# Kernel tuning notes

Hardware: AMD Instinct MI355X
Metric: run time of the kernel (lower is better)

## Reference

```python
import jax, jax.numpy as jnp
import numpy as np

N = 8192; S = 32; EMB = 256; NH = 8; HD = EMB // NH; NT = 4; K = 2; L = 2; E = 131072
IN_DIMS = [128, 64, 32, 16]; COUNTS = [4096, 2048, 1024, 1024]
BETA = 1.0; TEMPER = 1.0; SLOPE = 0.2; LN_EPS = 1e-5


def setup_inputs() -> dict:
    key = jax.random.key(0)
    ks = iter(jax.random.split(key, 64))
    def nrm(shape, scale=1.0):
        return jax.random.normal(next(ks), shape, jnp.float32) * scale
    inp = {}
    for i, (d, c) in enumerate(zip(IN_DIMS, COUNTS)):
        inp[f"feat{i}"] = nrm((c, d))
        inp[f"Wfc{i}"] = nrm((d, EMB), d ** -0.5)
        inp[f"bfc{i}"] = nrm((EMB,), 0.01)
    inp["type_emb"] = nrm((NT, NT))
    inp["Wgcn"] = nrm((K, EMB, EMB), EMB ** -0.5)
    inp["bgcn"] = nrm((K, EMB), 0.01)
    inp["Wre"] = nrm((K, NT, NT), NT ** -0.5)
    inp["bre"] = nrm((K, NT), 0.01)
    inp["wtre"] = jnp.ones((K, NT), jnp.float32)
    inp["Wl"] = nrm((L, EMB, EMB), EMB ** -0.5)
    inp["Wr"] = nrm((L, EMB, EMB), EMB ** -0.5)
    inp["al"] = nrm((L, HD), HD ** -0.5)
    inp["ar"] = nrm((L, HD), HD ** -0.5)
    inp["Wrs"] = nrm((L, NT, NT * NH), NT ** -0.5)
    inp["Wrt"] = nrm((L, NT, NT * NH), NT ** -0.5)
    inp["Wfin"] = nrm((L, EMB, EMB), EMB ** -0.5)
    inp["ln_g"] = jnp.ones((L, EMB), jnp.float32)
    inp["ln_b"] = jnp.zeros((L, EMB), jnp.float32)
    inp["src"] = jax.random.randint(next(ks), (E,), 0, N)
    inp["dst"] = jax.random.randint(next(ks), (E,), 0, N)
    inp["node_type"] = jnp.concatenate([jnp.full((c,), t, jnp.int32) for t, c in enumerate(COUNTS)])
    inp["seqs"] = jax.random.randint(next(ks), (N, S), 0, N)
    return inp


def _l2n(x):
    return x / jnp.maximum(jnp.linalg.norm(x, axis=1, keepdims=True), 1e-12)


def _ln(x, g, b):
    m = x.mean(-1, keepdims=True)
    v = ((x - m) ** 2).mean(-1, keepdims=True)
    return (x - m) * jax.lax.rsqrt(v + LN_EPS) * g + b


def _agt(h, rh, Wl_, Wr_, al_, ar_, Wrs_, Wrt_, Wfin_, g_, b_):
    B, Sq, _ = h.shape
    fl = (h @ Wl_).reshape(B, Sq, NH, HD).transpose(0, 2, 1, 3)  # [B,NH,S,HD]
    fr = (h @ Wr_).reshape(B, Sq, NH, HD).transpose(0, 2, 1, 3)
    sl = jnp.einsum('bhsd,d->bhs', jax.nn.leaky_relu(fl, SLOPE), al_)
    sr = jnp.einsum('bhsd,d->bhs', jax.nn.leaky_relu(fr, SLOPE), ar_)
    score = sl[:, :, :, None] + sr[:, :, None, :]  # [B,NH,S,S]
    rk = (rh @ Wrs_).reshape(B, Sq, NH, NT).transpose(0, 2, 1, 3)  # [B,NH,S,NT]
    rq = (rh @ Wrt_).reshape(B, Sq, NH, NT).transpose(0, 2, 1, 3)
    score = score + BETA * jnp.einsum('bhir,bhjr->bhij', rk, rq)
    attn = jax.nn.softmax(score / TEMPER, axis=-1)
    ctx = jnp.einsum('bhij,bhjd->bhid', attn, fr)
    h_sa = ctx.transpose(0, 2, 1, 3).reshape(B, Sq, EMB)
    return _ln(h + h_sa @ Wfin_, g_, b_)


def reference(feat0, feat1, feat2, feat3, Wfc0, bfc0, Wfc1, bfc1, Wfc2, bfc2, Wfc3, bfc3,
              type_emb, Wgcn, bgcn, Wre, bre, wtre, Wl, Wr, al, ar, Wrs, Wrt, Wfin, ln_g, ln_b,
              src, dst, node_type, seqs):
    feats = [feat0, feat1, feat2, feat3]
    Wfcs = [Wfc0, Wfc1, Wfc2, Wfc3]
    bfcs = [bfc0, bfc1, bfc2, bfc3]
    gh = jnp.concatenate([f @ W + b for f, W, b in zip(feats, Wfcs, bfcs)], axis=0)  # [N,EMB]
    Nn = gh.shape[0]
    loop = jnp.arange(Nn, dtype=src.dtype)  # self-loops (graph.add_self_loop)
    src_f = jnp.concatenate([src, loop]); dst_f = jnp.concatenate([dst, loop])
    ones = jnp.ones(src_f.shape[0], jnp.float32)
    outdeg = jnp.clip(jax.ops.segment_sum(ones, src_f, num_segments=Nn), 1.0)
    indeg = jnp.clip(jax.ops.segment_sum(ones, dst_f, num_segments=Nn), 1.0)
    n_out = outdeg ** -0.5; n_in = indeg ** -0.5
    ret = [_l2n(gh)]
    R = type_emb[node_type]  # [N,NT]
    for k in range(K):
        # GraphConv, norm='both', relu
        x = (gh * n_out[:, None]) @ Wgcn[k]
        gh = jax.nn.relu(jax.ops.segment_sum(x[src_f], dst_f, num_segments=Nn) * n_in[:, None] + bgcn[k])
        # REConv: left norm, weight, per-node type scale, scatter-sum, right norm, bias, relu
        r = ((R * n_out[:, None]) @ Wre[k]) * wtre[k][node_type][:, None]
        R = jax.nn.relu(jax.ops.segment_sum(r[src_f], dst_f, num_segments=Nn) * n_in[:, None] + bre[k])
    h = gh[seqs]   # [N,S,EMB]
    rh = R[seqs]   # [N,S,NT]
    for l in range(L):
        h = _agt(h, rh, Wl[l], Wr[l], al[l], ar[l], Wrs[l], Wrt[l], Wfin[l], ln_g[l], ln_b[l])
        ret.append(_l2n(h[:, 0, :]))
    return jnp.concatenate(ret, axis=1)  # [N, EMB*(1+L)]
```

## Files before the change

### kernel.cpp

```cpp
#include <hip/hip_runtime.h>
#include <hip/hip_bf16.h>
#include <cstdint>
#include <cstddef>

typedef unsigned short ushortT;
typedef unsigned int uintT;

using bf16x8 = __attribute__((ext_vector_type(8))) short;
using f32x4  = __attribute__((ext_vector_type(4))) float;

static constexpr int NN  = 8192;
static constexpr int EE  = 131072;
static constexpr float SLOPE  = 0.2f;
static constexpr float LN_EPS = 1e-5f;

#define DEVI __device__ __forceinline__

DEVI float red32(float v) {
  #pragma unroll
  for (int m = 16; m >= 1; m >>= 1) v += __shfl_xor(v, m, 64);
  return v;
}
DEVI float red64(float v) {
  #pragma unroll
  for (int m = 32; m >= 1; m >>= 1) v += __shfl_xor(v, m, 64);
  return v;
}
DEVI float max32(float v) {
  #pragma unroll
  for (int m = 16; m >= 1; m >>= 1) v = fmaxf(v, __shfl_xor(v, m, 64));
  return v;
}
DEVI float blo(uintT u) { union { uintT i; float f; } c; c.i = u << 16; return c.f; }
DEVI float bhi(uintT u) { union { uintT i; float f; } c; c.i = u & 0xffff0000u; return c.f; }
DEVI float b2f(ushortT u) { union { uintT i; float f; } c; c.i = ((uintT)u) << 16; return c.f; }
DEVI ushortT f2bu(float f) {
  __hip_bfloat16 h = __float2bfloat16(f);
  return *reinterpret_cast<ushortT*>(&h);
}
DEVI void storeC(float* p, float v) { *p = v; }
DEVI void storeC(ushortT* p, float v) { *p = f2bu(v); }

__global__ __launch_bounds__(256) void fc_kernel(
    const float* __restrict__ f0, const float* __restrict__ f1,
    const float* __restrict__ f2, const float* __restrict__ f3,
    const float* __restrict__ w0, const float* __restrict__ w1,
    const float* __restrict__ w2, const float* __restrict__ w3,
    const float* __restrict__ b0, const float* __restrict__ b1,
    const float* __restrict__ b2, const float* __restrict__ b3,
    float* __restrict__ gh, float* __restrict__ out)
{
  const int nb = blockIdx.x * 32;
  const int t  = threadIdx.x;
  int base, D;
  const float *F, *W, *Bv;
  if (nb < 4096)      { base = 0;    D = 128; F = f0; W = w0; Bv = b0; }
  else if (nb < 6144) { base = 4096; D = 64;  F = f1; W = w1; Bv = b1; }
  else if (nb < 7168) { base = 6144; D = 32;  F = f2; W = w2; Bv = b2; }
  else                { base = 7168; D = 16;  F = f3; W = w3; Bv = b3; }

  __shared__ float Fs[32 * 128];
  __shared__ float red[32][4];
  __shared__ float nrm[32];

  const int total = 32 * D;
  for (int i = t; i < total; i += 256) Fs[i] = F[(size_t)(nb - base) * D + i];
  __syncthreads();

  float acc[32];
  #pragma unroll
  for (int r = 0; r < 32; ++r) acc[r] = Bv[t];
  for (int d = 0; d < D; ++d) {
    float w = W[(size_t)d * 256 + t];
    #pragma unroll
    for (int r = 0; r < 32; ++r) acc[r] = fmaf(Fs[r * D + d], w, acc[r]);
  }

  const int lane = t & 63, wid = t >> 6;
  #pragma unroll
  for (int r = 0; r < 32; ++r) {
    float v = acc[r] * acc[r];
    for (int o = 32; o > 0; o >>= 1) v += __shfl_down(v, o, 64);
    if (lane == 0) red[r][wid] = v;
  }
  __syncthreads();
  if (t < 32) {
    float s = red[t][0] + red[t][1] + red[t][2] + red[t][3];
    nrm[t] = 1.0f / fmaxf(sqrtf(s), 1e-12f);
  }
  __syncthreads();
  #pragma unroll
  for (int r = 0; r < 32; ++r) {
    gh[(size_t)(nb + r) * 256 + t]  = acc[r];
    out[(size_t)(nb + r) * 768 + t] = acc[r] * nrm[r];
  }
}

__global__ __launch_bounds__(256) void zero_counts(int* outc, int* inc) {
  int g = blockIdx.x * 256 + threadIdx.x;
  if (g < NN) outc[g] = 0; else inc[g - NN] = 0;
}
__global__ __launch_bounds__(256) void count_deg(const int* __restrict__ src,
                                                 const int* __restrict__ dst,
                                                 int* outc, int* inc) {
  int g = blockIdx.x * 256 + threadIdx.x;
  atomicAdd(&outc[src[g]], 1);
  atomicAdd(&inc[dst[g]], 1);
}
__global__ __launch_bounds__(256) void norm_kernel(const int* __restrict__ outc,
                                                   const int* __restrict__ inc,
                                                   float* n_out, float* n_in) {
  int g = blockIdx.x * 256 + threadIdx.x;
  n_out[g] = rsqrtf((float)outc[g] + 1.0f);
  n_in[g]  = rsqrtf((float)inc[g] + 1.0f);
}
__global__ __launch_bounds__(1024) void scan_kernel(const int* __restrict__ inc,
                                                    int* __restrict__ offs) {
  __shared__ int sums[1024];
  const int t = threadIdx.x;
  int x[8];
  const int base = t * 8;
  int s = 0;
  #pragma unroll
  for (int i = 0; i < 8; ++i) { int v = inc[base + i] + 1; x[i] = s; s += v; }
  sums[t] = s;
  __syncthreads();
  for (int off = 1; off < 1024; off <<= 1) {
    int a = (t >= off) ? sums[t - off] : 0;
    __syncthreads();
    sums[t] += a;
    __syncthreads();
  }
  const int pre = (t > 0) ? sums[t - 1] : 0;
  #pragma unroll
  for (int i = 0; i < 8; ++i) offs[base + i] = pre + x[i];
  if (t == 1023) offs[NN] = sums[1023];
}
__global__ __launch_bounds__(256) void copy_cur(const int* __restrict__ offs, int* cur) {
  int g = blockIdx.x * 256 + threadIdx.x;
  cur[g] = offs[g];
}
__global__ __launch_bounds__(256) void fill_csr(const int* __restrict__ src,
                                                const int* __restrict__ dst,
                                                int* cur, int* __restrict__ csr) {
  int g = blockIdx.x * 256 + threadIdx.x;
  int s, d;
  if (g < EE) { s = src[g]; d = dst[g]; }
  else        { s = g - EE; d = g - EE; }
  int pos = atomicAdd(&cur[d], 1);
  csr[pos] = s;
}
__global__ __launch_bounds__(256) void init_R(const float* __restrict__ type_emb,
                                              const int* __restrict__ nt,
                                              float* __restrict__ R) {
  int g = blockIdx.x * 256 + threadIdx.x;
  int n = g >> 2, c = g & 3;
  R[g] = type_emb[nt[n] * 4 + c];
}

template<bool ROWSCALE, bool STORE, bool RED, typename CT>
__global__ __launch_bounds__(256) void mfma_gemm_kernel(
    const float* __restrict__ A, const float* __restrict__ W,
    const float* __restrict__ rowscale,
    CT* __restrict__ C, const float* __restrict__ avec,
    float* __restrict__ SSo)
{
  const int m0 = blockIdx.x * 64;
  const int n0 = blockIdx.y * 64;
  const int t = threadIdx.x;
  const int w = t >> 6, l = t & 63;
  const int wr = w >> 1, wc = w & 1;
  const int l15 = l & 15, l16 = l >> 4;

  __shared__ alignas(16) ushortT As[64][72];
  __shared__ alignas(16) ushortT Bs[64][72];

  f32x4 acc[2][2];
  #pragma unroll
  for (int mh = 0; mh < 2; ++mh)
    #pragma unroll
    for (int nh = 0; nh < 2; ++nh)
      #pragma unroll
      for (int r = 0; r < 4; ++r) acc[mh][nh][r] = 0.f;

  for (int k0 = 0; k0 < 256; k0 += 64) {
    #pragma unroll
    for (int rep = 0; rep < 16; ++rep) {
      int flat = rep * 256 + t;
      int r = flat >> 6, k = flat & 63;
      float v = A[(size_t)(m0 + r) * 256 + k0 + k];
      if constexpr (ROWSCALE) v *= rowscale[m0 + r];
      As[r][k] = f2bu(v);
    }
    #pragma unroll
    for (int rep = 0; rep < 16; ++rep) {
      int flat = rep * 256 + t;
      int k = flat >> 6, n = flat & 63;
      Bs[n][k] = f2bu(W[(size_t)(k0 + k) * 256 + n0 + n]);
    }
    __syncthreads();
    #pragma unroll
    for (int ks = 0; ks < 2; ++ks) {
      const int kb = ks * 32 + l16 * 8;
      bf16x8 afr[2], bfr[2];
      #pragma unroll
      for (int mh = 0; mh < 2; ++mh)
        afr[mh] = *reinterpret_cast<const bf16x8*>(&As[wr * 32 + mh * 16 + l15][kb]);
      #pragma unroll
      for (int nh = 0; nh < 2; ++nh)
        bfr[nh] = *reinterpret_cast<const bf16x8*>(&Bs[wc * 32 + nh * 16 + l15][kb]);
      #pragma unroll
      for (int mh = 0; mh < 2; ++mh)
        #pragma unroll
        for (int nh = 0; nh < 2; ++nh)
          acc[mh][nh] = __builtin_amdgcn_mfma_f32_16x16x32_bf16(
              afr[mh], bfr[nh], acc[mh][nh], 0, 0, 0);
    }
    __syncthreads();
  }
  if constexpr (STORE) {
    #pragma unroll
    for (int mh = 0; mh < 2; ++mh)
      #pragma unroll
      for (int nh = 0; nh < 2; ++nh)
        #pragma unroll
        for (int r = 0; r < 4; ++r) {
          const int row = m0 + wr * 32 + mh * 16 + l16 * 4 + r;
          const int col = n0 + wc * 32 + nh * 16 + l15;
          storeC(&C[(size_t)row * 256 + col], acc[mh][nh][r]);
        }
  }
  if constexpr (RED) {
    const float av0 = avec[l15], av1 = avec[16 + l15];
    #pragma unroll
    for (int mh = 0; mh < 2; ++mh)
      #pragma unroll
      for (int r = 0; r < 4; ++r) {
        float s = 0.f;
        {
          float x = acc[mh][0][r];
          s = fmaf(x > 0.f ? x : SLOPE * x, av0, s);
          x = acc[mh][1][r];
          s = fmaf(x > 0.f ? x : SLOPE * x, av1, s);
        }
        #pragma unroll
        for (int m = 8; m >= 1; m >>= 1) s += __shfl_xor(s, m, 64);
        if (l15 == 0) {
          const int row = m0 + wr * 32 + mh * 16 + l16 * 4 + r;
          SSo[(size_t)row * 8 + blockIdx.y * 2 + wc] = s;
        }
      }
  }
}

__global__ __launch_bounds__(256) void agg2_kernel(
    const int* __restrict__ offs, const int* __restrict__ csr,
    const ushortT* __restrict__ X, const float* __restrict__ n_in,
    const float* __restrict__ bias, float* __restrict__ ghn,
    ushortT* __restrict__ ghb)
{
  const int n  = blockIdx.x * 2 + (threadIdx.x >> 7);
  const int tc = threadIdx.x & 127;
  const uintT* X2 = reinterpret_cast<const uintT*>(X);
  const int s0 = offs[n], s1 = offs[n + 1];
  float a0 = 0.f, a1 = 0.f;
  for (int i = s0; i < s1; ++i) {
    const uintT u = X2[(size_t)csr[i] * 128 + tc];
    a0 += blo(u);
    a1 += bhi(u);
  }
  const float ni = n_in[n];
  const float g0 = fmaxf(fmaf(a0, ni, bias[2 * tc]), 0.f);
  const float g1 = fmaxf(fmaf(a1, ni, bias[2 * tc + 1]), 0.f);
  float2 g2; g2.x = g0; g2.y = g1;
  reinterpret_cast<float2*>(ghn)[(size_t)n * 128 + tc] = g2;
  if (ghb)
    reinterpret_cast<uintT*>(ghb)[(size_t)n * 128 + tc] =
        (uintT)f2bu(g0) | ((uintT)f2bu(g1) << 16);
}

__global__ __launch_bounds__(256) void re_proj(
    const float* __restrict__ R, const float* __restrict__ n_out,
    const float* __restrict__ Wre, const float* __restrict__ wtre,
    const int* __restrict__ nt, float* __restrict__ rtmp)
{
  int g = blockIdx.x * 256 + threadIdx.x;
  int n = g >> 2, j = g & 3;
  float s = 0.f;
  #pragma unroll
  for (int c = 0; c < 4; ++c) s += R[n * 4 + c] * Wre[c * 4 + j];
  rtmp[g] = s * n_out[n] * wtre[nt[n]];
}
__global__ __launch_bounds__(256) void re_agg(
    const int* __restrict__ offs, const int* __restrict__ csr,
    const float* __restrict__ rtmp, const float* __restrict__ n_in,
    const float* __restrict__ bre, float* __restrict__ Rn)
{
  int g = blockIdx.x * 256 + threadIdx.x;
  int n = g >> 2, j = g & 3;
  float a = 0.f;
  for (int i = offs[n]; i < offs[n + 1]; ++i) a += rtmp[csr[i] * 4 + j];
  Rn[g] = fmaxf(fmaf(a, n_in[n], bre[j]), 0.f);
}
__global__ __launch_bounds__(256) void rkq_kernel(
    const float* __restrict__ R, const float* __restrict__ Wrs,
    const float* __restrict__ Wrt, float* __restrict__ RKQ)
{
  int g = blockIdx.x * 256 + threadIdx.x;
  int n = g >> 7, c = g & 127;
  int which = c >> 5, cc = c & 31;
  const float* Wp = (which == 0) ? Wrs : (which == 1) ? Wrt
                   : (which == 2) ? (Wrs + 128) : (Wrt + 128);
  float s = 0.f;
  #pragma unroll
  for (int r = 0; r < 4; ++r) s += R[n * 4 + r] * Wp[r * 32 + cc];
  RKQ[g] = s;
}

__global__ __launch_bounds__(256) void vec4_kernel(
    const float* __restrict__ ln_g, const float* __restrict__ ln_b,
    const float* __restrict__ Wr2, float* __restrict__ vecs)
{
  const int which = blockIdx.x, t = threadIdx.x;
  const float* s = (which & 1) ? ln_b : ln_g;
  float a = 0.f;
  for (int k = 0; k < 256; ++k) a = fmaf(s[k], Wr2[(size_t)k * 256 + t], a);
  vecs[which * 256 + t] = a;
}
__global__ __launch_bounds__(256) void wg2i_kernel(
    const float* __restrict__ ln_g, const float* __restrict__ Wr2,
    ushortT* __restrict__ Wg2i)
{
  const int gid = blockIdx.x * 256 + threadIdx.x;
  const int ks  = gid >> 10;
  const int cgl = (gid >> 6) & 15;
  const int l   = gid & 63;
  const int col = cgl * 16 + (l & 15);
  const int kb  = ks * 32 + (l >> 4) * 8;
  ushortT v[8];
  #pragma unroll
  for (int e = 0; e < 8; ++e)
    v[e] = f2bu(ln_g[kb + e] * Wr2[(size_t)(kb + e) * 256 + col]);
  *reinterpret_cast<bf16x8*>(&Wg2i[(size_t)gid * 8]) =
      *reinterpret_cast<const bf16x8*>(v);
}
__global__ __launch_bounds__(256) void wl2b_kernel(
    const float* __restrict__ Wl2, ushortT* __restrict__ Wl2b)
{
  int g = blockIdx.x * 256 + threadIdx.x;
  Wl2b[g] = f2bu(Wl2[g]);
}

__global__ __launch_bounds__(256) void mega7_kernel(
    const int* __restrict__ seqs,
    const ushortT* __restrict__ ghb,
    const ushortT* __restrict__ GW,
    const float* __restrict__ SLg, const float* __restrict__ SRg,
    const float* __restrict__ RKQ,
    const float* __restrict__ vecs,
    const ushortT* __restrict__ Wg2i,
    const ushortT* __restrict__ Wl2b,
    const float* __restrict__ al2, const float* __restrict__ ar2,
    const float* __restrict__ ln_g, const float* __restrict__ ln_b,
    float* __restrict__ h1r0buf, float* __restrict__ ctx2buf,
    float* __restrict__ out)
{
  __shared__ int idx[32];
  __shared__ alignas(16) ushortT bufA[10240];
  __shared__ alignas(16) ushortT bufB[10240];
  __shared__ float SRs[8][32];
  __shared__ float RQs[32][36];
  __shared__ float rk2s[32];
  __shared__ float part[32][4], partq[32][4];
  __shared__ float mu_s[32], rs_s[32];
  __shared__ float SR2s[8][32];
  __shared__ float sl2s[8];
  __shared__ float scp[8][32];
  __shared__ float h1r0s[256];
  __shared__ float wred4[4];
  __shared__ float nrm1s;

  const int b = blockIdx.x, t = threadIdx.x;
  const int h8 = t >> 5, lo = t & 31;
  const int w = t >> 6, l = t & 63;
  const int l15 = l & 15, l16 = l >> 4;

  if (t < 32) idx[t] = seqs[b * 32 + t];
  __syncthreads();

  const float sli = SLg[(size_t)idx[lo] * 8 + h8];
  const float rk0 = RKQ[(size_t)idx[lo] * 128 + h8 * 4 + 0];
  const float rk1 = RKQ[(size_t)idx[lo] * 128 + h8 * 4 + 1];
  const float rk2_ = RKQ[(size_t)idx[lo] * 128 + h8 * 4 + 2];
  const float rk3 = RKQ[(size_t)idx[lo] * 128 + h8 * 4 + 3];

  {
    const uintT* GWu = reinterpret_cast<const uintT*>(GW);
    #pragma unroll
    for (int rep = 0; rep < 16; ++rep) {
      int flat = rep * 256 + t;
      int j = flat >> 7, cp = flat & 127;
      const uintT u = GWu[(size_t)idx[j] * 128 + cp];
      const int rA = 2 * cp;
      const int k = (rA >> 3) & 3;
      const int off = (((j >> 3) ^ k) << 3) + (j & 7);
      bufA[rA * 40 + off]       = (ushortT)(u & 0xffffu);
      bufA[(rA + 1) * 40 + off] = (ushortT)(u >> 16);
    }
  }
  SRs[h8][lo] = SRg[(size_t)idx[lo] * 8 + h8];
  #pragma unroll
  for (int rep = 0; rep < 4; ++rep) {
    int flat = rep * 256 + t, s3 = flat >> 5, c3 = flat & 31;
    RQs[s3][c3] = RKQ[(size_t)idx[s3] * 128 + 32 + c3];
  }
  if (t < 32) rk2s[t] = RKQ[(size_t)idx[0] * 128 + 64 + t];
  __syncthreads();

  {
    float p1[32];
    float m = -1e30f;
    #pragma unroll
    for (int j = 0; j < 32; ++j) {
      float sc = sli + SRs[h8][j]
               + rk0 * RQs[j][h8 * 4 + 0] + rk1 * RQs[j][h8 * 4 + 1]
               + rk2_ * RQs[j][h8 * 4 + 2] + rk3 * RQs[j][h8 * 4 + 3];
      p1[j] = sc; m = fmaxf(m, sc);
    }
    float sum = 0.f;
    #pragma unroll
    for (int j = 0; j < 32; ++j) { p1[j] = __expf(p1[j] - m); sum += p1[j]; }
    const float inv = 1.f / sum;
    const int row = t;
    const int k = (row >> 3) & 3;
    uintT* pw = reinterpret_cast<uintT*>(bufB) + row * 20;
    #pragma unroll
    for (int o = 0; o < 4; ++o) {
      uint4 v;
      v.x = (uintT)f2bu(p1[8 * o + 0] * inv) | ((uintT)f2bu(p1[8 * o + 1] * inv) << 16);
      v.y = (uintT)f2bu(p1[8 * o + 2] * inv) | ((uintT)f2bu(p1[8 * o + 3] * inv) << 16);
      v.z = (uintT)f2bu(p1[8 * o + 4] * inv) | ((uintT)f2bu(p1[8 * o + 5] * inv) << 16);
      v.w = (uintT)f2bu(p1[8 * o + 6] * inv) | ((uintT)f2bu(p1[8 * o + 7] * inv) << 16);
      *reinterpret_cast<uint4*>(pw + ((o ^ k) << 2)) = v;
    }
  }
  __syncthreads();

  int irow[2][4];
  #pragma unroll
  for (int mh = 0; mh < 2; ++mh)
    #pragma unroll
    for (int r = 0; r < 4; ++r)
      irow[mh][r] = idx[mh * 16 + l16 * 4 + r];

  bf16x8 af[2][2];
  #pragma unroll
  for (int hh = 0; hh < 2; ++hh) {
    const int h = 2 * w + hh;
    #pragma unroll
    for (int mh = 0; mh < 2; ++mh) {
      const int row = h * 32 + mh * 16 + l15;
      const int k = (row >> 3) & 3;
      af[hh][mh] = *reinterpret_cast<const bf16x8*>(&bufB[row * 40 + ((l16 ^ k) << 3)]);
    }
  }

  f32x4 acc[2][2][2];
  #pragma unroll
  for (int hh = 0; hh < 2; ++hh) {
    const int h = 2 * w + hh;
    bf16x8 bf[2];
    #pragma unroll
    for (int nh = 0; nh < 2; ++nh) {
      const int row = h * 32 + nh * 16 + l15;
      const int k = (row >> 3) & 3;
      bf[nh] = *reinterpret_cast<const bf16x8*>(&bufA[row * 40 + ((l16 ^ k) << 3)]);
    }
    #pragma unroll
    for (int mh = 0; mh < 2; ++mh)
      #pragma unroll
      for (int nh = 0; nh < 2; ++nh) {
        f32x4 z = {0.f, 0.f, 0.f, 0.f};
        acc[hh][mh][nh] = __builtin_amdgcn_mfma_f32_16x16x32_bf16(af[hh][mh], bf[nh], z, 0, 0, 0);
      }
  }
  {
    float sum_[2][4], sq_[2][4];
    #pragma unroll
    for (int mh = 0; mh < 2; ++mh)
      #pragma unroll
      for (int r = 0; r < 4; ++r) { sum_[mh][r] = 0.f; sq_[mh][r] = 0.f; }
    #pragma unroll
    for (int hh = 0; hh < 2; ++hh)
      #pragma unroll
      for (int mh = 0; mh < 2; ++mh)
        #pragma unroll
        for (int nh = 0; nh < 2; ++nh) {
          const int col = (2 * w + hh) * 32 + nh * 16 + l15;
          #pragma unroll
          for (int r = 0; r < 4; ++r) {
            float v = acc[hh][mh][nh][r] + b2f(ghb[(size_t)irow[mh][r] * 256 + col]);
            acc[hh][mh][nh][r] = v;
            sum_[mh][r] += v;
            sq_[mh][r] = fmaf(v, v, sq_[mh][r]);
          }
        }
    #pragma unroll
    for (int mh = 0; mh < 2; ++mh)
      #pragma unroll
      for (int r = 0; r < 4; ++r) {
        float s = sum_[mh][r], q = sq_[mh][r];
        #pragma unroll
        for (int m = 8; m >= 1; m >>= 1) {
          s += __shfl_xor(s, m, 64);
          q += __shfl_xor(q, m, 64);
        }
        if (l15 == 0) {
          part[mh * 16 + l16 * 4 + r][w]  = s;
          partq[mh * 16 + l16 * 4 + r][w] = q;
        }
      }
    if (l16 == 0) {
      #pragma unroll
      for (int hh = 0; hh < 2; ++hh)
        #pragma unroll
        for (int nh = 0; nh < 2; ++nh)
          h1r0s[(2 * w + hh) * 32 + nh * 16 + l15] = acc[hh][0][nh][0];
    }
  }
  __syncthreads();

  if (t < 32) {
    float sm = part[t][0] + part[t][1] + part[t][2] + part[t][3];
    float sq = partq[t][0] + partq[t][1] + partq[t][2] + partq[t][3];
    const float m = sm * (1.f / 256.f);
    const float v = fmaxf(sq * (1.f / 256.f) - m * m, 0.f);
    mu_s[t] = m;
    rs_s[t] = rsqrtf(v + LN_EPS);
  }
  __syncthreads();

  #pragma unroll
  for (int hh = 0; hh < 2; ++hh)
    #pragma unroll
    for (int mh = 0; mh < 2; ++mh)
      #pragma unroll
      for (int nh = 0; nh < 2; ++nh) {
        const int col = (2 * w + hh) * 32 + nh * 16 + l15;
        #pragma unroll
        for (int r = 0; r < 4; ++r) {
          const int row = mh * 16 + l16 * 4 + r;
          bufB[row * 264 + col] = f2bu(acc[hh][mh][nh][r]);
        }
      }
  #pragma unroll
  for (int rep = 0; rep < 4; ++rep) {
    int flat = rep * 256 + t, s3 = flat >> 5, c3 = flat & 31;
    RQs[s3][c3] = RKQ[(size_t)idx[s3] * 128 + 96 + c3];
  }
  {
    const float mu0 = mu_s[0], rs0 = rs_s[0];
    float hv = fmaf((h1r0s[t] - mu0) * rs0, ln_g[t], ln_b[t]);
    h1r0buf[(size_t)b * 256 + t] = hv;
    float sq = red64(hv * hv);
    h1r0s[t] = hv;
    if ((t & 63) == 0) wred4[t >> 6] = sq;
  }
  __syncthreads();

  if (t == 0) nrm1s = 1.f / fmaxf(sqrtf(wred4[0] + wred4[1] + wred4[2] + wred4[3]), 1e-12f);

  {
    f32x4 acc2[2][4];
    #pragma unroll
    for (int mh = 0; mh < 2; ++mh)
      #pragma unroll
      for (int cg = 0; cg < 4; ++cg)
        #pragma unroll
        for (int r = 0; r < 4; ++r) acc2[mh][cg][r] = 0.f;
    #pragma unroll
    for (int ks = 0; ks < 8; ++ks) {
      const int ko = ks * 32 + l16 * 8;
      bf16x8 a2[2];
      #pragma unroll
      for (int mh = 0; mh < 2; ++mh)
        a2[mh] = *reinterpret_cast<const bf16x8*>(&bufB[(mh * 16 + l15) * 264 + ko]);
      #pragma unroll
      for (int cg = 0; cg < 4; ++cg) {
        const bf16x8 b2 = *reinterpret_cast<const bf16x8*>(
            &Wg2i[((size_t)(ks * 16 + (w * 4 + cg)) * 64 + l) * 8]);
        #pragma unroll
        for (int mh = 0; mh < 2; ++mh)
          acc2[mh][cg] = __builtin_amdgcn_mfma_f32_16x16x32_bf16(a2[mh], b2, acc2[mh][cg], 0, 0, 0);
      }
    }
    float rsv[2][4], rmv[2][4];
    #pragma unroll
    for (int mh = 0; mh < 2; ++mh)
      #pragma unroll
      for (int r = 0; r < 4; ++r) {
        const int row = mh * 16 + l16 * 4 + r;
        rsv[mh][r] = rs_s[row];
        rmv[mh][r] = rsv[mh][r] * mu_s[row];
      }
    float sacc[2][2][4];
    #pragma unroll
    for (int hh = 0; hh < 2; ++hh)
      #pragma unroll
      for (int mh = 0; mh < 2; ++mh)
        #pragma unroll
        for (int r = 0; r < 4; ++r) sacc[hh][mh][r] = 0.f;
    float ar2v[2] = { ar2[l15], ar2[16 + l15] };
    #pragma unroll
    for (int cg = 0; cg < 4; ++cg) {
      const int col = w * 64 + cg * 16 + l15;
      const float v1c = vecs[col], v2c = vecs[256 + col];
      const int hh = cg >> 1;
      #pragma unroll
      for (int mh = 0; mh < 2; ++mh)
        #pragma unroll
        for (int r = 0; r < 4; ++r) {
          const int row = mh * 16 + l16 * 4 + r;
          float fa = fmaf(rsv[mh][r], acc2[mh][cg][r], fmaf(-rmv[mh][r], v1c, v2c));
          bufA[row * 268 + col] = f2bu(fa);
          float lr = fa > 0.f ? fa : SLOPE * fa;
          sacc[hh][mh][r] = fmaf(lr, ar2v[cg & 1], sacc[hh][mh][r]);
        }
    }
    #pragma unroll
    for (int hh = 0; hh < 2; ++hh)
      #pragma unroll
      for (int mh = 0; mh < 2; ++mh)
        #pragma unroll
        for (int r = 0; r < 4; ++r) {
          float s = sacc[hh][mh][r];
          #pragma unroll
          for (int m = 8; m >= 1; m >>= 1) s += __shfl_xor(s, m, 64);
          if (l15 == 0) SR2s[2 * w + hh][mh * 16 + l16 * 4 + r] = s;
        }
  }
  {
    float fl = 0.f;
    #pragma unroll 8
    for (int k = 0; k < 256; ++k)
      fl = fmaf(h1r0s[k], b2f(Wl2b[(size_t)k * 256 + t]), fl);
    float lr = (fl > 0.f ? fl : SLOPE * fl) * al2[lo];
    lr = red32(lr);
    if (lo == 0) sl2s[h8] = lr;
  }
  __syncthreads();

  {
    float s2 = sl2s[h8] + SR2s[h8][lo]
             + rk2s[h8 * 4 + 0] * RQs[lo][h8 * 4 + 0]
             + rk2s[h8 * 4 + 1] * RQs[lo][h8 * 4 + 1]
             + rk2s[h8 * 4 + 2] * RQs[lo][h8 * 4 + 2]
             + rk2s[h8 * 4 + 3] * RQs[lo][h8 * 4 + 3];
    const float m2 = max32(s2);
    const float e = __expf(s2 - m2);
    const float su = red32(e);
    scp[h8][lo] = e / su;
  }
  __syncthreads();

  {
    float a = 0.f;
    #pragma unroll
    for (int j = 0; j < 32; ++j) a = fmaf(scp[h8][j], b2f(bufA[j * 268 + t]), a);
    ctx2buf[(size_t)b * 256 + t] = a;
  }
  out[(size_t)b * 768 + 256 + t] = h1r0s[t] * nrm1s;
}

__global__ __launch_bounds__(256) void ln_l2n_kernel(
    const float* __restrict__ Y, const float* __restrict__ res,
    const float* __restrict__ lng, const float* __restrict__ lnb,
    float* __restrict__ out)
{
  const int row = blockIdx.x, t = threadIdx.x;
  __shared__ float s4[4], q4[4];
  const float y = Y[(size_t)row * 256 + t] + res[(size_t)row * 256 + t];
  float s = red64(y);
  float q = red64(y * y);
  if ((t & 63) == 0) { s4[t >> 6] = s; q4[t >> 6] = q; }
  __syncthreads();
  const float mu = (s4[0] + s4[1] + s4[2] + s4[3]) * (1.f / 256.f);
  const float var = fmaxf((q4[0] + q4[1] + q4[2] + q4[3]) * (1.f / 256.f) - mu * mu, 0.f);
  const float rstd = rsqrtf(var + LN_EPS);
  const float yn = fmaf((y - mu) * rstd, lng[t], lnb[t]);
  float nq = red64(yn * yn);
  __syncthreads();
  if ((t & 63) == 0) s4[t >> 6] = nq;
  __syncthreads();
  const float nrm = 1.f / fmaxf(sqrtf(s4[0] + s4[1] + s4[2] + s4[3]), 1e-12f);
  out[(size_t)row * 768 + 512 + t] = yn * nrm;
}

extern "C" void kernel_launch(void* const* d_in, const int* in_sizes, int n_in,
                              void* d_out, int out_size, void* d_ws, size_t ws_size,
                              hipStream_t stream)
{
  (void)in_sizes; (void)n_in; (void)out_size; (void)ws_size;

  const float* feat[4]; const float* wfc[4]; const float* bfc[4];
  for (int i = 0; i < 4; ++i) {
    feat[i] = (const float*)d_in[i * 3 + 0];
    wfc[i]  = (const float*)d_in[i * 3 + 1];
    bfc[i]  = (const float*)d_in[i * 3 + 2];
  }
  const float* type_emb = (const float*)d_in[12];
  const float* Wgcn = (const float*)d_in[13];
  const float* bgcn = (const float*)d_in[14];
  const float* Wre  = (const float*)d_in[15];
  const float* bre  = (const float*)d_in[16];
  const float* wtre = (const float*)d_in[17];
  const float* Wl   = (const float*)d_in[18];
  const float* Wr   = (const float*)d_in[19];
  const float* al   = (const float*)d_in[20];
  const float* ar   = (const float*)d_in[21];
  const float* Wrs  = (const float*)d_in[22];
  const float* Wrt  = (const float*)d_in[23];
  const float* Wfin = (const float*)d_in[24];
  const float* ln_g = (const float*)d_in[25];
  const float* ln_b = (const float*)d_in[26];
  const int* src       = (const int*)d_in[27];
  const int* dst       = (const int*)d_in[28];
  const int* node_type = (const int*)d_in[29];
  const int* seqs      = (const int*)d_in[30];
  float* out = (float*)d_out;

  char* p = (char*)d_ws;
  auto take = [&](size_t n) { char* q = p; p += (n + 255) & ~(size_t)255; return q; };
  float* gh    = (float*)take((size_t)NN * 256 * 4);
  float* Xf    = (float*)take((size_t)NN * 256 * 4);
  float* GR1   = (float*)take((size_t)NN * 256 * 4);
  float* RKQ   = (float*)take((size_t)NN * 128 * 4);
  float* SLg   = (float*)take((size_t)NN * 8 * 4);
  float* SRg   = (float*)take((size_t)NN * 8 * 4);
  float* n_out = (float*)take((size_t)NN * 4);
  float* n_in_ = (float*)take((size_t)NN * 4);
  int*   outc  = (int*)take((size_t)NN * 4);
  int*   inc   = (int*)take((size_t)NN * 4);
  int*   offs  = (int*)take((size_t)(NN + 1) * 4);
  int*   cur   = (int*)take((size_t)NN * 4);
  int*   csr   = (int*)take((size_t)(EE + NN) * 4);
  float* R     = (float*)take((size_t)NN * 4 * 4);
  float* rtmp  = (float*)take((size_t)NN * 4 * 4);
  ushortT* GW   = (ushortT*)take((size_t)NN * 256 * 2);
  ushortT* ghb  = (ushortT*)take((size_t)NN * 256 * 2);
  ushortT* Xb   = (ushortT*)take((size_t)NN * 256 * 2);
  ushortT* Wg2i = (ushortT*)take((size_t)131072 * 2);
  ushortT* Wl2b = (ushortT*)take((size_t)65536 * 2);
  float* vecs  = (float*)take((size_t)2 * 256 * 4);
  float* ctx2buf = Xf;
  float* h1r0buf = GR1;
  float* Yb      = gh;

  const float* Wr2 = Wr + 65536;
  const float* Wl2 = Wl + 65536;

  fc_kernel<<<256, 256, 0, stream>>>(feat[0], feat[1], feat[2], feat[3],
                                     wfc[0], wfc[1], wfc[2], wfc[3],
                                     bfc[0], bfc[1], bfc[2], bfc[3], gh, out);
  zero_counts<<<64, 256, 0, stream>>>(outc, inc);
  count_deg<<<512, 256, 0, stream>>>(src, dst, outc, inc);
  norm_kernel<<<32, 256, 0, stream>>>(outc, inc, n_out, n_in_);
  scan_kernel<<<1, 1024, 0, stream>>>(inc, offs);
  copy_cur<<<32, 256, 0, stream>>>(offs, cur);
  fill_csr<<<544, 256, 0, stream>>>(src, dst, cur, csr);
  init_R<<<128, 256, 0, stream>>>(type_emb, node_type, R);

  vec4_kernel<<<2, 256, 0, stream>>>(ln_g, ln_b, Wr2, vecs);
  wg2i_kernel<<<64, 256, 0, stream>>>(ln_g, Wr2, Wg2i);
  wl2b_kernel<<<256, 256, 0, stream>>>(Wl2, Wl2b);

  for (int k = 0; k < 2; ++k) {
    mfma_gemm_kernel<true, true, false, ushortT>
        <<<dim3(128, 4), 256, 0, stream>>>(gh, Wgcn + (size_t)k * 65536,
                                           n_out, Xb, nullptr, nullptr);
    agg2_kernel<<<NN / 2, 256, 0, stream>>>(offs, csr, Xb, n_in_,
                                            bgcn + k * 256, gh,
                                            k == 1 ? ghb : nullptr);
    re_proj<<<128, 256, 0, stream>>>(R, n_out, Wre + k * 16, wtre + k * 4, node_type, rtmp);
    re_agg<<<128, 256, 0, stream>>>(offs, csr, rtmp, n_in_, bre + k * 4, R);
  }

  rkq_kernel<<<4096, 256, 0, stream>>>(R, Wrs, Wrt, RKQ);
  mfma_gemm_kernel<false, false, true, float>
      <<<dim3(128, 4), 256, 0, stream>>>(gh, Wl, nullptr, (float*)nullptr, al, SLg);
  mfma_gemm_kernel<false, true, true, float>
      <<<dim3(128, 4), 256, 0, stream>>>(gh, Wr, nullptr, GR1, ar, SRg);
  mfma_gemm_kernel<false, true, false, ushortT>
      <<<dim3(128, 4), 256, 0, stream>>>(GR1, Wfin, nullptr, GW, nullptr, nullptr);

  mega7_kernel<<<NN, 256, 0, stream>>>(seqs, ghb, GW, SLg, SRg, RKQ, vecs,
                                       Wg2i, Wl2b,
                                       al + 32, ar + 32, ln_g, ln_b,
                                       h1r0buf, ctx2buf, out);

  mfma_gemm_kernel<false, true, false, float>
      <<<dim3(128, 4), 256, 0, stream>>>(ctx2buf, Wfin + 65536, nullptr,
                                         Yb, nullptr, nullptr);
  ln_l2n_kernel<<<NN, 256, 0, stream>>>(Yb, h1r0buf, ln_g + 256, ln_b + 256, out);
}
```

Before: 572.7 us.

## Fuse final Wfin GEMM and LayerNorm into mega kernel; merge Wl/Wr GEMMs and small setup kernels

The final layer's Wfin projection, residual add, LayerNorm and L2 normalisation move into the per-sequence mega kernel. Each block does a 256x256 matrix-vector product in FP32 FMAs against bf16 weights, which removes the separate MFMA GEMM, the LN kernel and their intermediate buffers. The Wl and Wr projections become one MFMA kernel that shares the A tile, and norm and copy_cur are folded into the scan kernel. The cost is that every mega-kernel block now streams the whole 128KB Wfin2 matrix through a scalar matvec. This is likely served from L2, but it adds serial compute to each block.

```diff
diff --git a/kernel.cpp b/kernel.cpp
--- a/kernel.cpp
+++ b/kernel.cpp
@@ -107,15 +107,11 @@
   atomicAdd(&outc[src[g]], 1);
   atomicAdd(&inc[dst[g]], 1);
 }
-__global__ __launch_bounds__(256) void norm_kernel(const int* __restrict__ outc,
-                                                   const int* __restrict__ inc,
-                                                   float* n_out, float* n_in) {
-  int g = blockIdx.x * 256 + threadIdx.x;
-  n_out[g] = rsqrtf((float)outc[g] + 1.0f);
-  n_in[g]  = rsqrtf((float)inc[g] + 1.0f);
-}
-__global__ __launch_bounds__(1024) void scan_kernel(const int* __restrict__ inc,
-                                                    int* __restrict__ offs) {
+__global__ __launch_bounds__(1024) void scan_kernel(
+    const int* __restrict__ inc, const int* __restrict__ outc,
+    int* __restrict__ offs, int* __restrict__ cur,
+    float* __restrict__ n_out, float* __restrict__ n_in)
+{
   __shared__ int sums[1024];
   const int t = threadIdx.x;
   int x[8];
@@ -133,12 +129,14 @@
   }
   const int pre = (t > 0) ? sums[t - 1] : 0;
   #pragma unroll
-  for (int i = 0; i < 8; ++i) offs[base + i] = pre + x[i];
+  for (int i = 0; i < 8; ++i) {
+    const int o = pre + x[i];
+    offs[base + i] = o;
+    cur[base + i]  = o;
+    n_in[base + i]  = rsqrtf((float)inc[base + i] + 1.0f);
+    n_out[base + i] = rsqrtf((float)outc[base + i] + 1.0f);
+  }
   if (t == 1023) offs[NN] = sums[1023];
-}
-__global__ __launch_bounds__(256) void copy_cur(const int* __restrict__ offs, int* cur) {
-  int g = blockIdx.x * 256 + threadIdx.x;
-  cur[g] = offs[g];
 }
 __global__ __launch_bounds__(256) void fill_csr(const int* __restrict__ src,
                                                 const int* __restrict__ dst,
@@ -253,6 +251,111 @@
   }
 }
 
+__global__ __launch_bounds__(256) void mfma_wlwr_kernel(
+    const float* __restrict__ A,
+    const float* __restrict__ Wl_, const float* __restrict__ Wr_,
+    float* __restrict__ GR1,
+    const float* __restrict__ al_, const float* __restrict__ ar_,
+    float* __restrict__ SL, float* __restrict__ SR)
+{
+  const int m0 = blockIdx.x * 64;
+  const int n0 = blockIdx.y * 64;
+  const int t = threadIdx.x;
+  const int w = t >> 6, l = t & 63;
+  const int wr = w >> 1, wc = w & 1;
+  const int l15 = l & 15, l16 = l >> 4;
+
+  __shared__ alignas(16) ushortT As[64][72];
+  __shared__ alignas(16) ushortT Bl[64][72];
+  __shared__ alignas(16) ushortT Br[64][72];
+
+  f32x4 accl[2][2], accr[2][2];
+  #pragma unroll
+  for (int mh = 0; mh < 2; ++mh)
+    #pragma unroll
+    for (int nh = 0; nh < 2; ++nh)
+      #pragma unroll
+      for (int r = 0; r < 4; ++r) { accl[mh][nh][r] = 0.f; accr[mh][nh][r] = 0.f; }
+
+  for (int k0 = 0; k0 < 256; k0 += 64) {
+    #pragma unroll
+    for (int rep = 0; rep < 16; ++rep) {
+      int flat = rep * 256 + t;
+      int r = flat >> 6, k = flat & 63;
+      As[r][k] = f2bu(A[(size_t)(m0 + r) * 256 + k0 + k]);
+    }
+    #pragma unroll
+    for (int rep = 0; rep < 16; ++rep) {
+      int flat = rep * 256 + t;
+      int k = flat >> 6, n = flat & 63;
+      Bl[n][k] = f2bu(Wl_[(size_t)(k0 + k) * 256 + n0 + n]);
+      Br[n][k] = f2bu(Wr_[(size_t)(k0 + k) * 256 + n0 + n]);
+    }
+    __syncthreads();
+    #pragma unroll
+    for (int ks = 0; ks < 2; ++ks) {
+      const int kb = ks * 32 + l16 * 8;
+      bf16x8 afr[2], blr[2], brr[2];
+      #pragma unroll
+      for (int mh = 0; mh < 2; ++mh)
+        afr[mh] = *reinterpret_cast<const bf16x8*>(&As[wr * 32 + mh * 16 + l15][kb]);
+      #pragma unroll
+      for (int nh = 0; nh < 2; ++nh) {
+        blr[nh] = *reinterpret_cast<const bf16x8*>(&Bl[wc * 32 + nh * 16 + l15][kb]);
+        brr[nh] = *reinterpret_cast<const bf16x8*>(&Br[wc * 32 + nh * 16 + l15][kb]);
+      }
+      #pragma unroll
+      for (int mh = 0; mh < 2; ++mh)
+        #pragma unroll
+        for (int nh = 0; nh < 2; ++nh) {
+          accl[mh][nh] = __builtin_amdgcn_mfma_f32_16x16x32_bf16(
+              afr[mh], blr[nh], accl[mh][nh], 0, 0, 0);
+          accr[mh][nh] = __builtin_amdgcn_mfma_f32_16x16x32_bf16(
+              afr[mh], brr[nh], accr[mh][nh], 0, 0, 0);
+        }
+    }
+    __syncthreads();
+  }
+  #pragma unroll
+  for (int mh = 0; mh < 2; ++mh)
+    #pragma unroll
+    for (int nh = 0; nh < 2; ++nh)
+      #pragma unroll
+      for (int r = 0; r < 4; ++r) {
+        const int row = m0 + wr * 32 + mh * 16 + l16 * 4 + r;
+        const int col = n0 + wc * 32 + nh * 16 + l15;
+        GR1[(size_t)row * 256 + col] = accr[mh][nh][r];
+      }
+  const float al0 = al_[l15], al1 = al_[16 + l15];
+  const float ar0 = ar_[l15], ar1 = ar_[16 + l15];
+  #pragma unroll
+  for (int mh = 0; mh < 2; ++mh)
+    #pragma unroll
+    for (int r = 0; r < 4; ++r) {
+      float sl = 0.f, sr = 0.f;
+      {
+        float x = accl[mh][0][r];
+        sl = fmaf(x > 0.f ? x : SLOPE * x, al0, sl);
+        x = accl[mh][1][r];
+        sl = fmaf(x > 0.f ? x : SLOPE * x, al1, sl);
+        x = accr[mh][0][r];
+        sr = fmaf(x > 0.f ? x : SLOPE * x, ar0, sr);
+        x = accr[mh][1][r];
+        sr = fmaf(x > 0.f ? x : SLOPE * x, ar1, sr);
+      }
+      #pragma unroll
+      for (int m = 8; m >= 1; m >>= 1) {
+        sl += __shfl_xor(sl, m, 64);
+        sr += __shfl_xor(sr, m, 64);
+      }
+      if (l15 == 0) {
+        const int row = m0 + wr * 32 + mh * 16 + l16 * 4 + r;
+        SL[(size_t)row * 8 + blockIdx.y * 2 + wc] = sl;
+        SR[(size_t)row * 8 + blockIdx.y * 2 + wc] = sr;
+      }
+    }
+}
+
 __global__ __launch_bounds__(256) void agg2_kernel(
     const int* __restrict__ offs, const int* __restrict__ csr,
     const ushortT* __restrict__ X, const float* __restrict__ n_in,
@@ -344,14 +447,16 @@
   *reinterpret_cast<bf16x8*>(&Wg2i[(size_t)gid * 8]) =
       *reinterpret_cast<const bf16x8*>(v);
 }
-__global__ __launch_bounds__(256) void wl2b_kernel(
-    const float* __restrict__ Wl2, ushortT* __restrict__ Wl2b)
+__global__ __launch_bounds__(256) void wcvt_kernel(
+    const float* __restrict__ Wl2, const float* __restrict__ Wfin2,
+    ushortT* __restrict__ Wl2b, ushortT* __restrict__ Wf2b)
 {
   int g = blockIdx.x * 256 + threadIdx.x;
-  Wl2b[g] = f2bu(Wl2[g]);
-}
-
-__global__ __launch_bounds__(256) void mega7_kernel(
+  if (g < 65536) Wl2b[g] = f2bu(Wl2[g]);
+  else { int q = g - 65536; Wf2b[q] = f2bu(Wfin2[q]); }
+}
+
+__global__ __launch_bounds__(256) void mega8_kernel(
     const int* __restrict__ seqs,
     const ushortT* __restrict__ ghb,
     const ushortT* __restrict__ GW,
@@ -360,9 +465,9 @@
     const float* __restrict__ vecs,
     const ushortT* __restrict__ Wg2i,
     const ushortT* __restrict__ Wl2b,
+    const ushortT* __restrict__ Wf2b,
     const float* __restrict__ al2, const float* __restrict__ ar2,
     const float* __restrict__ ln_g, const float* __restrict__ ln_b,
-    float* __restrict__ h1r0buf, float* __restrict__ ctx2buf,
     float* __restrict__ out)
 {
   __shared__ int idx[32];
@@ -377,6 +482,7 @@
   __shared__ float sl2s[8];
   __shared__ float scp[8][32];
   __shared__ float h1r0s[256];
+  __shared__ float ctx2s[256];
   __shared__ float wred4[4];
   __shared__ float nrm1s;
 
@@ -561,7 +667,6 @@
   {
     const float mu0 = mu_s[0], rs0 = rs_s[0];
     float hv = fmaf((h1r0s[t] - mu0) * rs0, ln_g[t], ln_b[t]);
-    h1r0buf[(size_t)b * 256 + t] = hv;
     float sq = red64(hv * hv);
     h1r0s[t] = hv;
     if ((t & 63) == 0) wred4[t >> 6] = sq;
@@ -667,33 +772,31 @@
     float a = 0.f;
     #pragma unroll
     for (int j = 0; j < 32; ++j) a = fmaf(scp[h8][j], b2f(bufA[j * 268 + t]), a);
-    ctx2buf[(size_t)b * 256 + t] = a;
+    ctx2s[t] = a;
   }
   out[(size_t)b * 768 + 256 + t] = h1r0s[t] * nrm1s;
-}
-
-__global__ __launch_bounds__(256) void ln_l2n_kernel(
-    const float* __restrict__ Y, const float* __restrict__ res,
-    const float* __restrict__ lng, const float* __restrict__ lnb,
-    float* __restrict__ out)
-{
-  const int row = blockIdx.x, t = threadIdx.x;
-  __shared__ float s4[4], q4[4];
-  const float y = Y[(size_t)row * 256 + t] + res[(size_t)row * 256 + t];
-  float s = red64(y);
-  float q = red64(y * y);
-  if ((t & 63) == 0) { s4[t >> 6] = s; q4[t >> 6] = q; }
-  __syncthreads();
-  const float mu = (s4[0] + s4[1] + s4[2] + s4[3]) * (1.f / 256.f);
-  const float var = fmaxf((q4[0] + q4[1] + q4[2] + q4[3]) * (1.f / 256.f) - mu * mu, 0.f);
-  const float rstd = rsqrtf(var + LN_EPS);
-  const float yn = fmaf((y - mu) * rstd, lng[t], lnb[t]);
-  float nq = red64(yn * yn);
-  __syncthreads();
-  if ((t & 63) == 0) s4[t >> 6] = nq;
-  __syncthreads();
-  const float nrm = 1.f / fmaxf(sqrtf(s4[0] + s4[1] + s4[2] + s4[3]), 1e-12f);
-  out[(size_t)row * 768 + 512 + t] = yn * nrm;
+  __syncthreads();
+
+  {
+    float yv = 0.f;
+    #pragma unroll 8
+    for (int k = 0; k < 256; ++k)
+      yv = fmaf(ctx2s[k], b2f(Wf2b[(size_t)k * 256 + t]), yv);
+    const float y = yv + h1r0s[t];
+    float s = red64(y);
+    float q = red64(y * y);
+    if ((t & 63) == 0) { part[0][t >> 6] = s; partq[0][t >> 6] = q; }
+    __syncthreads();
+    const float mu = (part[0][0] + part[0][1] + part[0][2] + part[0][3]) * (1.f / 256.f);
+    const float var = fmaxf((partq[0][0] + partq[0][1] + partq[0][2] + partq[0][3]) * (1.f / 256.f) - mu * mu, 0.f);
+    const float rstd = rsqrtf(var + LN_EPS);
+    const float yn = fmaf((y - mu) * rstd, ln_g[256 + t], ln_b[256 + t]);
+    float nq = red64(yn * yn);
+    if ((t & 63) == 0) part[1][t >> 6] = nq;
+    __syncthreads();
+    const float nrm = 1.f / fmaxf(sqrtf(part[1][0] + part[1][1] + part[1][2] + part[1][3]), 1e-12f);
+    out[(size_t)b * 768 + 512 + t] = yn * nrm;
+  }
 }
 
 extern "C" void kernel_launch(void* const* d_in, const int* in_sizes, int n_in,
@@ -732,7 +835,6 @@
   char* p = (char*)d_ws;
   auto take = [&](size_t n) { char* q = p; p += (n + 255) & ~(size_t)255; return q; };
   float* gh    = (float*)take((size_t)NN * 256 * 4);
-  float* Xf    = (float*)take((size_t)NN * 256 * 4);
   float* GR1   = (float*)take((size_t)NN * 256 * 4);
   float* RKQ   = (float*)take((size_t)NN * 128 * 4);
   float* SLg   = (float*)take((size_t)NN * 8 * 4);
@@ -751,10 +853,8 @@
   ushortT* Xb   = (ushortT*)take((size_t)NN * 256 * 2);
   ushortT* Wg2i = (ushortT*)take((size_t)131072 * 2);
   ushortT* Wl2b = (ushortT*)take((size_t)65536 * 2);
+  ushortT* Wf2b = (ushortT*)take((size_t)65536 * 2);
   float* vecs  = (float*)take((size_t)2 * 256 * 4);
-  float* ctx2buf = Xf;
-  float* h1r0buf = GR1;
-  float* Yb      = gh;
 
   const float* Wr2 = Wr + 65536;
   const float* Wl2 = Wl + 65536;
@@ -764,15 +864,13 @@
                                      bfc[0], bfc[1], bfc[2], bfc[3], gh, out);
   zero_counts<<<64, 256, 0, stream>>>(outc, inc);
   count_deg<<<512, 256, 0, stream>>>(src, dst, outc, inc);
-  norm_kernel<<<32, 256, 0, stream>>>(outc, inc, n_out, n_in_);
-  scan_kernel<<<1, 1024, 0, stream>>>(inc, offs);
-  copy_cur<<<32, 256, 0, stream>>>(offs, cur);
+  scan_kernel<<<1, 1024, 0, stream>>>(inc, outc, offs, cur, n_out, n_in_);
   fill_csr<<<544, 256, 0, stream>>>(src, dst, cur, csr);
   init_R<<<128, 256, 0, stream>>>(type_emb, node_type, R);
 
   vec4_kernel<<<2, 256, 0, stream>>>(ln_g, ln_b, Wr2, vecs);
   wg2i_kernel<<<64, 256, 0, stream>>>(ln_g, Wr2, Wg2i);
-  wl2b_kernel<<<256, 256, 0, stream>>>(Wl2, Wl2b);
+  wcvt_kernel<<<512, 256, 0, stream>>>(Wl2, Wfin + 65536, Wl2b, Wf2b);
 
   for (int k = 0; k < 2; ++k) {
     mfma_gemm_kernel<true, true, false, ushortT>
@@ -786,20 +884,12 @@
   }
 
   rkq_kernel<<<4096, 256, 0, stream>>>(R, Wrs, Wrt, RKQ);
-  mfma_gemm_kernel<false, false, true, float>
-      <<<dim3(128, 4), 256, 0, stream>>>(gh, Wl, nullptr, (float*)nullptr, al, SLg);
-  mfma_gemm_kernel<false, true, true, float>
-      <<<dim3(128, 4), 256, 0, stream>>>(gh, Wr, nullptr, GR1, ar, SRg);
+  mfma_wlwr_kernel<<<dim3(128, 4), 256, 0, stream>>>(
+      gh, Wl, Wr, GR1, al, ar, SLg, SRg);
   mfma_gemm_kernel<false, true, false, ushortT>
       <<<dim3(128, 4), 256, 0, stream>>>(GR1, Wfin, nullptr, GW, nullptr, nullptr);
 
-  mega7_kernel<<<NN, 256, 0, stream>>>(seqs, ghb, GW, SLg, SRg, RKQ, vecs,
-                                       Wg2i, Wl2b,
-                                       al + 32, ar + 32, ln_g, ln_b,
-                                       h1r0buf, ctx2buf, out);
-
-  mfma_gemm_kernel<false, true, false, float>
-      <<<dim3(128, 4), 256, 0, stream>>>(ctx2buf, Wfin + 65536, nullptr,
-                                         Yb, nullptr, nullptr);
-  ln_l2n_kernel<<<NN, 256, 0, stream>>>(Yb, h1r0buf, ln_g + 256, ln_b + 256, out);
-}
+  mega8_kernel<<<NN, 256, 0, stream>>>(seqs, ghb, GW, SLg, SRg, RKQ, vecs,
+                                       Wg2i, Wl2b, Wf2b,
+                                       al + 32, ar + 32, ln_g, ln_b, out);
+}
```

New measurement: 601.1 us. 1.05x slower.
